# Performance work log

Hardware: AMD Instinct MI355X
Metric: run time of the kernel (lower is better)

## Reference

```python
import jax, jax.numpy as jnp
import numpy as np

N = 50000        # nodes
E = 1_600_000    # edges
R = 4            # relations
F_IN = 32        # input_size
H1 = 32          # 8 * multiplier
H2 = 64          # 16 * multiplier
NC = 3           # num_classes
G = 64           # graphs in batch


def setup_inputs() -> dict:
    key = jax.random.key(0)
    ks = jax.random.split(key, 16)
    s = 0.1
    x = jax.random.normal(ks[0], (N, F_IN), jnp.float32)
    edge_index = jax.random.randint(ks[1], (2, E), 0, N, dtype=jnp.int32)
    edge_type = jax.random.randint(ks[2], (E,), 0, R, dtype=jnp.int32)
    batch = jnp.sort(jax.random.randint(ks[3], (N,), 0, G, dtype=jnp.int32))
    return {
        "x": x,
        "edge_index": edge_index,
        "edge_type": edge_type,
        "batch": batch,
        # RGCNConv 1: per-relation weights, root weight, bias
        "W1_rel": jax.random.normal(ks[4], (R, F_IN, H1), jnp.float32) * s,
        "W1_root": jax.random.normal(ks[5], (F_IN, H1), jnp.float32) * s,
        "b1": jax.random.normal(ks[6], (H1,), jnp.float32) * s,
        # RGCNConv 2
        "W2_rel": jax.random.normal(ks[7], (R, H1, H2), jnp.float32) * s,
        "W2_root": jax.random.normal(ks[8], (H1, H2), jnp.float32) * s,
        "b2": jax.random.normal(ks[9], (H2,), jnp.float32) * s,
        # MLP head (stored as (in, out))
        "lin1_w": jax.random.normal(ks[10], (H2, H1), jnp.float32) * s,
        "lin1_b": jax.random.normal(ks[11], (H1,), jnp.float32) * s,
        "lin2_w": jax.random.normal(ks[12], (H1, NC), jnp.float32) * s,
        "lin2_b": jax.random.normal(ks[13], (NC,), jnp.float32) * s,
    }


def _rgcn_layer(x, src, dst, edge_type, W_rel, W_root, b):
    # PyG RGCNConv: out_i = x_i @ W_root + b + sum_r mean_{j in N_r(i)} x_j @ W_r
    out = x @ W_root + b
    for r in range(R):  # small fixed relation count
        h = x @ W_rel[r]                       # [N, out] dense transform once per relation
        mask = (edge_type == r)
        msg = jnp.where(mask[:, None], h[src], 0.0)          # [E, out] masked gather
        agg = jax.ops.segment_sum(msg, dst, num_segments=N)  # [N, out]
        cnt = jax.ops.segment_sum(mask.astype(x.dtype), dst, num_segments=N)
        out = out + agg / jnp.maximum(cnt, 1.0)[:, None]     # mean aggregation
    return out


def reference(x, edge_index, edge_type, batch, W1_rel, W1_root, b1,
              W2_rel, W2_root, b2, lin1_w, lin1_b, lin2_w, lin2_b):
    src, dst = edge_index[0], edge_index[1]
    h = jax.nn.relu(_rgcn_layer(x, src, dst, edge_type, W1_rel, W1_root, b1))
    h = jax.nn.relu(_rgcn_layer(h, src, dst, edge_type, W2_rel, W2_root, b2))
    g = jax.ops.segment_max(h, batch, num_segments=G)        # global_max_pool -> [G, H2]
    g = jnp.where(jnp.isneginf(g), 0.0, g)                   # empty-graph guard
    g = jax.nn.relu(g @ lin1_w + lin1_b)
    return g @ lin2_w + lin2_b
```

## Files before the change

### kernel.cpp

```cpp
#include <hip/hip_runtime.h>

#define N_NODES 50000
#define N_EDGES 1600000
#define R_REL 4
#define F_IN 32
#define H1 32
#define H2 64
#define NC 3
#define G_BATCH 64
#define BKT 196
#define CHUNK 6400
#define NBIN (N_EDGES / CHUNK)
#define ELIST_CAP (N_EDGES + N_NODES * R_REL * 8)

__global__ __launch_bounds__(256) void copyx_kernel(const float* __restrict__ x,
                                                    float* __restrict__ xp,
                                                    float* __restrict__ h1zero) {
    int i = blockIdx.x * 256 + threadIdx.x;
    if (i < (N_NODES + 1) * F_IN)
        xp[i] = (i < N_NODES * F_IN) ? x[i] : 0.0f;
    if (i < H1) h1zero[i] = 0.0f;
}

__global__ __launch_bounds__(256) void bcount_kernel(const int* __restrict__ dstp,
                                                     int* __restrict__ bucketCnt) {
    __shared__ int h[BKT];
    for (int i = threadIdx.x; i < BKT; i += 256) h[i] = 0;
    __syncthreads();
    int e0 = blockIdx.x * CHUNK;
    for (int e = e0 + threadIdx.x; e < e0 + CHUNK; e += 256)
        atomicAdd(&h[dstp[e] >> 8], 1);
    __syncthreads();
    for (int i = threadIdx.x; i < BKT; i += 256)
        if (h[i]) atomicAdd(&bucketCnt[i], h[i]);
}

__global__ __launch_bounds__(256) void bscan_kernel(const int* __restrict__ bucketCnt,
                                                    int* __restrict__ bucketOff,
                                                    int* __restrict__ bucketCursor) {
    __shared__ int s[256];
    int v = (threadIdx.x < BKT) ? bucketCnt[threadIdx.x] : 0;
    s[threadIdx.x] = v;
    __syncthreads();
    for (int w = 1; w < 256; w <<= 1) {
        int t = (threadIdx.x >= w) ? s[threadIdx.x - w] : 0;
        __syncthreads();
        s[threadIdx.x] += t;
        __syncthreads();
    }
    if (threadIdx.x < BKT) {
        int o = s[threadIdx.x] - v;
        bucketOff[threadIdx.x] = o;
        bucketCursor[threadIdx.x] = o;
    }
}

__global__ __launch_bounds__(256) void bin_kernel(const int* __restrict__ srcp,
                                                  const int* __restrict__ dstp,
                                                  const int* __restrict__ etype,
                                                  int* __restrict__ bucketCursor,
                                                  int* __restrict__ binned) {
    __shared__ int h[BKT];
    __shared__ int lc[BKT];
    for (int i = threadIdx.x; i < BKT; i += 256) { h[i] = 0; lc[i] = 0; }
    __syncthreads();
    int e0 = blockIdx.x * CHUNK;
    for (int e = e0 + threadIdx.x; e < e0 + CHUNK; e += 256)
        atomicAdd(&h[dstp[e] >> 8], 1);
    __syncthreads();
    for (int i = threadIdx.x; i < BKT; i += 256) {
        int c = h[i];
        h[i] = c ? atomicAdd(&bucketCursor[i], c) : 0;
    }
    __syncthreads();
    for (int e = e0 + threadIdx.x; e < e0 + CHUNK; e += 256) {
        int d = dstp[e];
        int b = d >> 8;
        int rank = atomicAdd(&lc[b], 1);
        binned[h[b] + rank] = srcp[e] | (etype[e] << 16) | ((d & 0xFF) << 18);
    }
}

__global__ __launch_bounds__(256) void bcnt2_kernel(const int* __restrict__ binned,
                                                    const int* __restrict__ bucketOff,
                                                    const int* __restrict__ bucketCnt,
                                                    float* __restrict__ inv,
                                                    int* __restrict__ rcnt4,
                                                    int* __restrict__ partial) {
    __shared__ int cnt4[256 * R_REL];
    __shared__ int s[256];
    for (int i = threadIdx.x; i < 256 * R_REL; i += 256) cnt4[i] = 0;
    __syncthreads();
    int b = blockIdx.x;
    int i0 = bucketOff[b], i1 = i0 + bucketCnt[b];
    for (int i = i0 + threadIdx.x; i < i1; i += 256) {
        int p = binned[i];
        atomicAdd(&cnt4[((p >> 18) & 0xFF) * R_REL + ((p >> 16) & 3)], 1);
    }
    __syncthreads();
    int n = b * 256 + threadIdx.x;
    int d = 0;
    if (n < N_NODES) {
        int4 w;
        int c0 = cnt4[threadIdx.x * 4 + 0];
        int c1 = cnt4[threadIdx.x * 4 + 1];
        int c2 = cnt4[threadIdx.x * 4 + 2];
        int c3 = cnt4[threadIdx.x * 4 + 3];
        inv[0 * N_NODES + n] = 1.0f / (float)(c0 > 1 ? c0 : 1);
        inv[1 * N_NODES + n] = 1.0f / (float)(c1 > 1 ? c1 : 1);
        inv[2 * N_NODES + n] = 1.0f / (float)(c2 > 1 ? c2 : 1);
        inv[3 * N_NODES + n] = 1.0f / (float)(c3 > 1 ? c3 : 1);
        w.x = c0; w.y = c1; w.z = c2; w.w = c3;
        *(int4*)&rcnt4[n * 4] = w;
        d = ((c0 + 7) & ~7) + ((c1 + 7) & ~7) + ((c2 + 7) & ~7) + ((c3 + 7) & ~7);
    }
    s[threadIdx.x] = d;
    __syncthreads();
    for (int w = 128; w > 0; w >>= 1) {
        if (threadIdx.x < w) s[threadIdx.x] += s[threadIdx.x + w];
        __syncthreads();
    }
    if (threadIdx.x == 0) partial[b] = s[0];
}

__global__ __launch_bounds__(256) void scanB_kernel(int* __restrict__ partial) {
    __shared__ int s[256];
    int v = (threadIdx.x < BKT) ? partial[threadIdx.x] : 0;
    s[threadIdx.x] = v;
    __syncthreads();
    for (int w = 1; w < 256; w <<= 1) {
        int t = (threadIdx.x >= w) ? s[threadIdx.x - w] : 0;
        __syncthreads();
        s[threadIdx.x] += t;
        __syncthreads();
    }
    if (threadIdx.x < BKT) partial[threadIdx.x] = s[threadIdx.x] - v;
}

__global__ __launch_bounds__(256) void scanC_kernel(const int* __restrict__ rcnt4,
                                                    const int* __restrict__ partial,
                                                    int* __restrict__ poff4) {
    __shared__ int s[256];
    int n = blockIdx.x * 256 + threadIdx.x;
    int p0 = 0, p1 = 0, p2 = 0, p3 = 0, d = 0;
    if (n < N_NODES) {
        int4 rc = *(const int4*)&rcnt4[n * 4];
        p0 = (rc.x + 7) & ~7;
        p1 = (rc.y + 7) & ~7;
        p2 = (rc.z + 7) & ~7;
        p3 = (rc.w + 7) & ~7;
        d = p0 + p1 + p2 + p3;
    }
    s[threadIdx.x] = d;
    __syncthreads();
    for (int w = 1; w < 256; w <<= 1) {
        int t = (threadIdx.x >= w) ? s[threadIdx.x - w] : 0;
        __syncthreads();
        s[threadIdx.x] += t;
        __syncthreads();
    }
    if (n < N_NODES) {
        int base = partial[blockIdx.x] + s[threadIdx.x] - d;
        int4 w;
        w.x = base;
        w.y = base + p0;
        w.z = base + p0 + p1;
        w.w = base + p0 + p1 + p2;
        *(int4*)&poff4[n * 4] = w;
    }
}

__global__ __launch_bounds__(256) void bscatter_kernel(const int* __restrict__ binned,
                                                       const int* __restrict__ bucketOff,
                                                       const int* __restrict__ bucketCnt,
                                                       const int* __restrict__ poff4,
                                                       const int* __restrict__ rcnt4,
                                                       int* __restrict__ elist) {
    __shared__ int cur[256 * 4];
    int b = blockIdx.x, t = threadIdx.x;
    int n = b * 256 + t;
    int4 po = make_int4(0, 0, 0, 0);
    if (n < N_NODES) po = *(const int4*)&poff4[n * 4];
    cur[t * 4 + 0] = po.x;
    cur[t * 4 + 1] = po.y;
    cur[t * 4 + 2] = po.z;
    cur[t * 4 + 3] = po.w;
    __syncthreads();
    int i0 = bucketOff[b], i1 = i0 + bucketCnt[b];
    for (int i = i0 + t; i < i1; i += 256) {
        int p = binned[i];
        int pos = atomicAdd(&cur[((p >> 18) & 0xFF) * 4 + ((p >> 16) & 3)], 1);
        elist[pos] = p & 0xFFFF;
    }
    __syncthreads();
    if (n < N_NODES) {
        int4 rc = *(const int4*)&rcnt4[n * 4];
        int rcv[4] = {rc.x, rc.y, rc.z, rc.w};
        int pov[4] = {po.x, po.y, po.z, po.w};
#pragma unroll
        for (int r = 0; r < R_REL; ++r) {
            int e = cur[t * 4 + r];
            int pe = pov[r] + ((rcv[r] + 7) & ~7);
            for (; e < pe; ++e) elist[e] = N_NODES;
        }
    }
}

__global__ __launch_bounds__(256, 8) void layer1_kernel(
    const float* __restrict__ xp, const int* __restrict__ poff4,
    const int* __restrict__ rcnt4, const int* __restrict__ elist,
    const float* __restrict__ inv, const float* __restrict__ W_rel,
    const float* __restrict__ W_root, const float* __restrict__ b,
    float* __restrict__ h1) {
    __shared__ float sxr[8][F_IN];
    __shared__ float sagg[8][R_REL][F_IN];

    int ln = threadIdx.x >> 5, c = threadIdx.x & 31;
    int n = blockIdx.x * 8 + ln;
    if (n >= N_NODES) return;

    sxr[ln][c] = xp[n * F_IN + c];
    int4 po = *(const int4*)&poff4[n * 4];
    int4 rc = *(const int4*)&rcnt4[n * 4];
    int pov[4] = {po.x, po.y, po.z, po.w};
    int rcv[4] = {rc.x, rc.y, rc.z, rc.w};
    int c7 = c & 7;
#pragma unroll
    for (int r = 0; r < R_REL; ++r) {
        int sb = pov[r];
        int pc = (rcv[r] + 7) & ~7;
        float a = 0.0f;
        for (int eb = 0; eb < pc; eb += 8) {
            int pv = elist[sb + eb + c7];
            float v[8];
#pragma unroll
            for (int j = 0; j < 8; ++j) {
                int p = __shfl(pv, j, 8);
                v[j] = xp[p * F_IN + c];
            }
#pragma unroll
            for (int j = 0; j < 8; ++j) a += v[j];
        }
        sagg[ln][r][c] = a * inv[r * N_NODES + n];
    }

    float o = b[c];
#pragma unroll
    for (int i = 0; i < F_IN; ++i)
        o = fmaf(sxr[ln][i], W_root[i * H1 + c], o);
#pragma unroll
    for (int r = 0; r < R_REL; ++r)
#pragma unroll
        for (int i = 0; i < F_IN; ++i)
            o = fmaf(sagg[ln][r][i], W_rel[r * F_IN * H1 + i * H1 + c], o);
    h1[n * H1 + c] = fmaxf(o, 0.0f);
}

__global__ __launch_bounds__(256, 8) void layer2_kernel(
    const float* __restrict__ h1, const int* __restrict__ poff4,
    const int* __restrict__ rcnt4, const int* __restrict__ elist,
    const float* __restrict__ inv, const float* __restrict__ W_rel,
    const float* __restrict__ W_root, const float* __restrict__ b,
    float* __restrict__ out2) {
    __shared__ float sxr[8][H1];
    __shared__ float sagg[8][R_REL][H1];

    int ln = threadIdx.x >> 5, c = threadIdx.x & 31;
    int n = blockIdx.x * 8 + ln;
    if (n >= N_NODES) return;

    sxr[ln][c] = h1[n * H1 + c];
    int4 po = *(const int4*)&poff4[n * 4];
    int4 rc = *(const int4*)&rcnt4[n * 4];
    int pov[4] = {po.x, po.y, po.z, po.w};
    int rcv[4] = {rc.x, rc.y, rc.z, rc.w};
    int c7 = c & 7;
#pragma unroll
    for (int r = 0; r < R_REL; ++r) {
        int sb = pov[r];
        int pc = (rcv[r] + 7) & ~7;
        float a = 0.0f;
        for (int eb = 0; eb < pc; eb += 8) {
            int pv = elist[sb + eb + c7];
            float v[8];
#pragma unroll
            for (int j = 0; j < 8; ++j) {
                int p = __shfl(pv, j, 8);
                v[j] = h1[p * H1 + c];
            }
#pragma unroll
            for (int j = 0; j < 8; ++j) a += v[j];
        }
        sagg[ln][r][c] = a * inv[r * N_NODES + n];
    }

    float o0 = b[c], o1 = b[c + 32];
#pragma unroll
    for (int i = 0; i < H1; ++i) {
        float xv = sxr[ln][i];
        o0 = fmaf(xv, W_root[i * H2 + c], o0);
        o1 = fmaf(xv, W_root[i * H2 + c + 32], o1);
    }
#pragma unroll
    for (int r = 0; r < R_REL; ++r)
#pragma unroll
        for (int i = 0; i < H1; ++i) {
            float av = sagg[ln][r][i];
            o0 = fmaf(av, W_rel[r * H1 * H2 + i * H2 + c], o0);
            o1 = fmaf(av, W_rel[r * H1 * H2 + i * H2 + c + 32], o1);
        }
    out2[n * H2 + c] = o0;
    out2[n * H2 + c + 32] = o1;
}

#define POOL_NODES 32
__global__ __launch_bounds__(64) void pool_kernel(
    const float* __restrict__ out2, const int* __restrict__ batch,
    unsigned int* __restrict__ g) {
    int col = threadIdx.x;
    int n0 = blockIdx.x * POOL_NODES;
    if (n0 >= N_NODES) return;
    int n1 = n0 + POOL_NODES;
    if (n1 > N_NODES) n1 = N_NODES;
    int cur = batch[n0];
    float m = 0.0f;
    for (int n = n0; n < n1; ++n) {
        int bnow = batch[n];
        if (bnow != cur) {
            atomicMax(&g[cur * H2 + col], __float_as_uint(m));
            cur = bnow;
            m = 0.0f;
        }
        m = fmaxf(m, out2[n * H2 + col]);
    }
    atomicMax(&g[cur * H2 + col], __float_as_uint(m));
}

__global__ __launch_bounds__(256) void mlp_kernel(
    const unsigned int* __restrict__ gbits, const float* __restrict__ lin1_w,
    const float* __restrict__ lin1_b, const float* __restrict__ lin2_w,
    const float* __restrict__ lin2_b, float* __restrict__ out) {
    __shared__ float sg[G_BATCH][H2];
    __shared__ float sh[G_BATCH][H1];
    __shared__ float sw1[H2 * H1];
    for (int i = threadIdx.x; i < G_BATCH * H2; i += 256)
        sg[i / H2][i % H2] = __uint_as_float(gbits[i]);
    for (int i = threadIdx.x; i < H2 * H1; i += 256) sw1[i] = lin1_w[i];
    __syncthreads();
    for (int i = threadIdx.x; i < G_BATCH * H1; i += 256) {
        int gi = i / H1, c = i % H1;
        float a = lin1_b[c];
#pragma unroll
        for (int k = 0; k < H2; ++k) a = fmaf(sg[gi][k], sw1[k * H1 + c], a);
        sh[gi][c] = fmaxf(a, 0.0f);
    }
    __syncthreads();
    for (int i = threadIdx.x; i < G_BATCH * NC; i += 256) {
        int gi = i / NC, c = i % NC;
        float a = lin2_b[c];
#pragma unroll
        for (int k = 0; k < H1; ++k) a = fmaf(sh[gi][k], lin2_w[k * NC + c], a);
        out[gi * NC + c] = a;
    }
}

extern "C" void kernel_launch(void* const* d_in, const int* in_sizes, int n_in,
                              void* d_out, int out_size, void* d_ws, size_t ws_size,
                              hipStream_t stream) {
    const float* x       = (const float*)d_in[0];
    const int*   eidx    = (const int*)d_in[1];
    const int*   etype   = (const int*)d_in[2];
    const int*   batch   = (const int*)d_in[3];
    const float* W1_rel  = (const float*)d_in[4];
    const float* W1_root = (const float*)d_in[5];
    const float* b1      = (const float*)d_in[6];
    const float* W2_rel  = (const float*)d_in[7];
    const float* W2_root = (const float*)d_in[8];
    const float* b2      = (const float*)d_in[9];
    const float* lin1_w  = (const float*)d_in[10];
    const float* lin1_b  = (const float*)d_in[11];
    const float* lin2_w  = (const float*)d_in[12];
    const float* lin2_b  = (const float*)d_in[13];
    const int* srcp = eidx;
    const int* dstp = eidx + N_EDGES;

    char* ws = (char*)d_ws;
    size_t o = 0;
    int*      bucketCnt    = (int*)(ws + o);   o += (size_t)256 * 4;
    int*      bucketOff    = (int*)(ws + o);   o += (size_t)256 * 4;
    int*      bucketCursor = (int*)(ws + o);   o += (size_t)256 * 4;
    int*      partial      = (int*)(ws + o);   o += (size_t)256 * 4;
    float*    inv          = (float*)(ws + o); o += (size_t)R_REL * N_NODES * 4;
    int*      rcnt4        = (int*)(ws + o);   o += (size_t)R_REL * N_NODES * 4;
    int*      poff4        = (int*)(ws + o);   o += (size_t)R_REL * N_NODES * 4;
    int*      binned       = (int*)(ws + o);   o += (size_t)N_EDGES * 4;
    int*      elist        = (int*)(ws + o);   o += (size_t)ELIST_CAP * 4;
    unsigned* g            = (unsigned*)(ws + o); o += (size_t)G_BATCH * H2 * 4;
    float*    xp           = (float*)(ws + o); o += (size_t)(N_NODES + 1) * F_IN * 4;
    float*    h1           = (float*)(ws + o); o += (size_t)(N_NODES + 1) * H1 * 4;
    float*    out2         = (float*)(ws + o); o += (size_t)N_NODES * H2 * 4;

    hipMemsetAsync(bucketCnt, 0, 256 * 4, stream);
    hipMemsetAsync(g, 0, (size_t)G_BATCH * H2 * 4, stream);

    copyx_kernel<<<((N_NODES + 1) * F_IN + 255) / 256, 256, 0, stream>>>(
        x, xp, h1 + (size_t)N_NODES * H1);
    bcount_kernel<<<NBIN, 256, 0, stream>>>(dstp, bucketCnt);
    bscan_kernel<<<1, 256, 0, stream>>>(bucketCnt, bucketOff, bucketCursor);
    bin_kernel<<<NBIN, 256, 0, stream>>>(srcp, dstp, etype, bucketCursor, binned);
    bcnt2_kernel<<<BKT, 256, 0, stream>>>(binned, bucketOff, bucketCnt, inv,
                                          rcnt4, partial);
    scanB_kernel<<<1, 256, 0, stream>>>(partial);
    scanC_kernel<<<BKT, 256, 0, stream>>>(rcnt4, partial, poff4);
    bscatter_kernel<<<BKT, 256, 0, stream>>>(binned, bucketOff, bucketCnt, poff4,
                                             rcnt4, elist);

    layer1_kernel<<<(N_NODES + 7) / 8, 256, 0, stream>>>(
        xp, poff4, rcnt4, elist, inv, W1_rel, W1_root, b1, h1);
    layer2_kernel<<<(N_NODES + 7) / 8, 256, 0, stream>>>(
        h1, poff4, rcnt4, elist, inv, W2_rel, W2_root, b2, out2);

    pool_kernel<<<(N_NODES + POOL_NODES - 1) / POOL_NODES, 64, 0, stream>>>(
        out2, batch, g);
    mlp_kernel<<<1, 256, 0, stream>>>(g, lin1_w, lin1_b, lin2_w, lin2_b,
                                      (float*)d_out);
}
```

Baseline: 320.1 us.

## Gather neighbors with one wavefront per node using float4 loads across relations

Layer kernels now assign a full 64-lane wavefront per node instead of 32 lanes. The wavefront processes 8 edges at once with float4 feature loads, and all four relations are interleaved in a single loop padded to the max count, followed by a cross-lane shuffle reduction. The layer-1 dense transform is split across the two half-waves. This is meant to raise memory-level parallelism and cut per-edge shuffle overhead in the gather, at the cost of wasted padded loads when relation counts differ. The edge-binning chunk size is also reduced to launch more blocks, and the elist gets extra slack for the over-read.

```diff
diff --git a/kernel.cpp b/kernel.cpp
--- a/kernel.cpp
+++ b/kernel.cpp
@@ -9,7 +9,7 @@
 #define NC 3
 #define G_BATCH 64
 #define BKT 196
-#define CHUNK 6400
+#define CHUNK 1600
 #define NBIN (N_EDGES / CHUNK)
 #define ELIST_CAP (N_EDGES + N_NODES * R_REL * 8)
 
@@ -206,111 +206,140 @@
     }
 }
 
+__device__ __forceinline__ void red4(float4& a) {
+#pragma unroll
+    for (int st = 8; st < 64; st <<= 1) {
+        a.x += __shfl_xor(a.x, st);
+        a.y += __shfl_xor(a.y, st);
+        a.z += __shfl_xor(a.z, st);
+        a.w += __shfl_xor(a.w, st);
+    }
+}
+__device__ __forceinline__ void acc4(float4& a, const float4 v) {
+    a.x += v.x; a.y += v.y; a.z += v.z; a.w += v.w;
+}
+
 __global__ __launch_bounds__(256, 8) void layer1_kernel(
     const float* __restrict__ xp, const int* __restrict__ poff4,
     const int* __restrict__ rcnt4, const int* __restrict__ elist,
     const float* __restrict__ inv, const float* __restrict__ W_rel,
-    const float* __restrict__ W_root, const float* __restrict__ b,
+    const float* __restrict__ W_root, const float* __restrict__ bb,
     float* __restrict__ h1) {
-    __shared__ float sxr[8][F_IN];
-    __shared__ float sagg[8][R_REL][F_IN];
-
-    int ln = threadIdx.x >> 5, c = threadIdx.x & 31;
-    int n = blockIdx.x * 8 + ln;
+    __shared__ float sxr[4][F_IN];
+    __shared__ float sagg[4][R_REL][F_IN];
+    int wid = threadIdx.x >> 6, lane = threadIdx.x & 63;
+    int n = blockIdx.x * 4 + wid;
     if (n >= N_NODES) return;
-
-    sxr[ln][c] = xp[n * F_IN + c];
+    int s = lane >> 3, q = lane & 7;
     int4 po = *(const int4*)&poff4[n * 4];
     int4 rc = *(const int4*)&rcnt4[n * 4];
-    int pov[4] = {po.x, po.y, po.z, po.w};
-    int rcv[4] = {rc.x, rc.y, rc.z, rc.w};
-    int c7 = c & 7;
-#pragma unroll
-    for (int r = 0; r < R_REL; ++r) {
-        int sb = pov[r];
-        int pc = (rcv[r] + 7) & ~7;
-        float a = 0.0f;
-        for (int eb = 0; eb < pc; eb += 8) {
-            int pv = elist[sb + eb + c7];
-            float v[8];
-#pragma unroll
-            for (int j = 0; j < 8; ++j) {
-                int p = __shfl(pv, j, 8);
-                v[j] = xp[p * F_IN + c];
-            }
-#pragma unroll
-            for (int j = 0; j < 8; ++j) a += v[j];
-        }
-        sagg[ln][r][c] = a * inv[r * N_NODES + n];
-    }
-
-    float o = b[c];
-#pragma unroll
-    for (int i = 0; i < F_IN; ++i)
-        o = fmaf(sxr[ln][i], W_root[i * H1 + c], o);
+    int pc0 = (rc.x + 7) & ~7, pc1 = (rc.y + 7) & ~7;
+    int pc2 = (rc.z + 7) & ~7, pc3 = (rc.w + 7) & ~7;
+    int mx = max(max(pc0, pc1), max(pc2, pc3));
+    if (lane < 8)
+        *(float4*)&sxr[wid][lane * 4] = *(const float4*)&xp[n * F_IN + lane * 4];
+
+    float4 a0 = {0, 0, 0, 0}, a1 = a0, a2 = a0, a3 = a0;
+    for (int eb = 0; eb < mx; eb += 8) {
+        int t0 = elist[po.x + eb + s];
+        int t1 = elist[po.y + eb + s];
+        int t2 = elist[po.z + eb + s];
+        int t3 = elist[po.w + eb + s];
+        int p0 = (eb < pc0) ? t0 : N_NODES;
+        int p1 = (eb < pc1) ? t1 : N_NODES;
+        int p2 = (eb < pc2) ? t2 : N_NODES;
+        int p3 = (eb < pc3) ? t3 : N_NODES;
+        acc4(a0, *(const float4*)&xp[p0 * F_IN + q * 4]);
+        acc4(a1, *(const float4*)&xp[p1 * F_IN + q * 4]);
+        acc4(a2, *(const float4*)&xp[p2 * F_IN + q * 4]);
+        acc4(a3, *(const float4*)&xp[p3 * F_IN + q * 4]);
+    }
+    red4(a0); red4(a1); red4(a2); red4(a3);
+    if (lane < 8) {
+        float s0 = inv[0 * N_NODES + n], s1 = inv[1 * N_NODES + n];
+        float s2 = inv[2 * N_NODES + n], s3 = inv[3 * N_NODES + n];
+        a0.x *= s0; a0.y *= s0; a0.z *= s0; a0.w *= s0;
+        a1.x *= s1; a1.y *= s1; a1.z *= s1; a1.w *= s1;
+        a2.x *= s2; a2.y *= s2; a2.z *= s2; a2.w *= s2;
+        a3.x *= s3; a3.y *= s3; a3.z *= s3; a3.w *= s3;
+        *(float4*)&sagg[wid][0][lane * 4] = a0;
+        *(float4*)&sagg[wid][1][lane * 4] = a1;
+        *(float4*)&sagg[wid][2][lane * 4] = a2;
+        *(float4*)&sagg[wid][3][lane * 4] = a3;
+    }
+    int col = lane & 31, half = lane >> 5, ib = half * 16;
+    float o = (half == 0) ? bb[col] : 0.0f;
+#pragma unroll
+    for (int k = 0; k < 16; ++k)
+        o = fmaf(sxr[wid][ib + k], W_root[(ib + k) * H1 + col], o);
 #pragma unroll
     for (int r = 0; r < R_REL; ++r)
 #pragma unroll
-        for (int i = 0; i < F_IN; ++i)
-            o = fmaf(sagg[ln][r][i], W_rel[r * F_IN * H1 + i * H1 + c], o);
-    h1[n * H1 + c] = fmaxf(o, 0.0f);
+        for (int k = 0; k < 16; ++k)
+            o = fmaf(sagg[wid][r][ib + k],
+                     W_rel[r * F_IN * H1 + (ib + k) * H1 + col], o);
+    o += __shfl_xor(o, 32);
+    if (half == 0) h1[n * H1 + col] = fmaxf(o, 0.0f);
 }
 
 __global__ __launch_bounds__(256, 8) void layer2_kernel(
     const float* __restrict__ h1, const int* __restrict__ poff4,
     const int* __restrict__ rcnt4, const int* __restrict__ elist,
     const float* __restrict__ inv, const float* __restrict__ W_rel,
-    const float* __restrict__ W_root, const float* __restrict__ b,
+    const float* __restrict__ W_root, const float* __restrict__ bb,
     float* __restrict__ out2) {
-    __shared__ float sxr[8][H1];
-    __shared__ float sagg[8][R_REL][H1];
-
-    int ln = threadIdx.x >> 5, c = threadIdx.x & 31;
-    int n = blockIdx.x * 8 + ln;
+    __shared__ float sxr[4][H1];
+    __shared__ float sagg[4][R_REL][H1];
+    int wid = threadIdx.x >> 6, lane = threadIdx.x & 63;
+    int n = blockIdx.x * 4 + wid;
     if (n >= N_NODES) return;
-
-    sxr[ln][c] = h1[n * H1 + c];
+    int s = lane >> 3, q = lane & 7;
     int4 po = *(const int4*)&poff4[n * 4];
     int4 rc = *(const int4*)&rcnt4[n * 4];
-    int pov[4] = {po.x, po.y, po.z, po.w};
-    int rcv[4] = {rc.x, rc.y, rc.z, rc.w};
-    int c7 = c & 7;
-#pragma unroll
-    for (int r = 0; r < R_REL; ++r) {
-        int sb = pov[r];
-        int pc = (rcv[r] + 7) & ~7;
-        float a = 0.0f;
-        for (int eb = 0; eb < pc; eb += 8) {
-            int pv = elist[sb + eb + c7];
-            float v[8];
-#pragma unroll
-            for (int j = 0; j < 8; ++j) {
-                int p = __shfl(pv, j, 8);
-                v[j] = h1[p * H1 + c];
-            }
-#pragma unroll
-            for (int j = 0; j < 8; ++j) a += v[j];
-        }
-        sagg[ln][r][c] = a * inv[r * N_NODES + n];
-    }
-
-    float o0 = b[c], o1 = b[c + 32];
-#pragma unroll
-    for (int i = 0; i < H1; ++i) {
-        float xv = sxr[ln][i];
-        o0 = fmaf(xv, W_root[i * H2 + c], o0);
-        o1 = fmaf(xv, W_root[i * H2 + c + 32], o1);
-    }
+    int pc0 = (rc.x + 7) & ~7, pc1 = (rc.y + 7) & ~7;
+    int pc2 = (rc.z + 7) & ~7, pc3 = (rc.w + 7) & ~7;
+    int mx = max(max(pc0, pc1), max(pc2, pc3));
+    if (lane < 8)
+        *(float4*)&sxr[wid][lane * 4] = *(const float4*)&h1[n * H1 + lane * 4];
+
+    float4 a0 = {0, 0, 0, 0}, a1 = a0, a2 = a0, a3 = a0;
+    for (int eb = 0; eb < mx; eb += 8) {
+        int t0 = elist[po.x + eb + s];
+        int t1 = elist[po.y + eb + s];
+        int t2 = elist[po.z + eb + s];
+        int t3 = elist[po.w + eb + s];
+        int p0 = (eb < pc0) ? t0 : N_NODES;
+        int p1 = (eb < pc1) ? t1 : N_NODES;
+        int p2 = (eb < pc2) ? t2 : N_NODES;
+        int p3 = (eb < pc3) ? t3 : N_NODES;
+        acc4(a0, *(const float4*)&h1[p0 * H1 + q * 4]);
+        acc4(a1, *(const float4*)&h1[p1 * H1 + q * 4]);
+        acc4(a2, *(const float4*)&h1[p2 * H1 + q * 4]);
+        acc4(a3, *(const float4*)&h1[p3 * H1 + q * 4]);
+    }
+    red4(a0); red4(a1); red4(a2); red4(a3);
+    if (lane < 8) {
+        float s0 = inv[0 * N_NODES + n], s1 = inv[1 * N_NODES + n];
+        float s2 = inv[2 * N_NODES + n], s3 = inv[3 * N_NODES + n];
+        a0.x *= s0; a0.y *= s0; a0.z *= s0; a0.w *= s0;
+        a1.x *= s1; a1.y *= s1; a1.z *= s1; a1.w *= s1;
+        a2.x *= s2; a2.y *= s2; a2.z *= s2; a2.w *= s2;
+        a3.x *= s3; a3.y *= s3; a3.z *= s3; a3.w *= s3;
+        *(float4*)&sagg[wid][0][lane * 4] = a0;
+        *(float4*)&sagg[wid][1][lane * 4] = a1;
+        *(float4*)&sagg[wid][2][lane * 4] = a2;
+        *(float4*)&sagg[wid][3][lane * 4] = a3;
+    }
+    float o = bb[lane];
+#pragma unroll
+    for (int i = 0; i < H1; ++i)
+        o = fmaf(sxr[wid][i], W_root[i * H2 + lane], o);
 #pragma unroll
     for (int r = 0; r < R_REL; ++r)
 #pragma unroll
-        for (int i = 0; i < H1; ++i) {
-            float av = sagg[ln][r][i];
-            o0 = fmaf(av, W_rel[r * H1 * H2 + i * H2 + c], o0);
-            o1 = fmaf(av, W_rel[r * H1 * H2 + i * H2 + c + 32], o1);
-        }
-    out2[n * H2 + c] = o0;
-    out2[n * H2 + c + 32] = o1;
+        for (int i = 0; i < H1; ++i)
+            o = fmaf(sagg[wid][r][i], W_rel[r * H1 * H2 + i * H2 + lane], o);
+    out2[n * H2 + lane] = o;
 }
 
 #define POOL_NODES 32
@@ -394,7 +423,7 @@
     int*      rcnt4        = (int*)(ws + o);   o += (size_t)R_REL * N_NODES * 4;
     int*      poff4        = (int*)(ws + o);   o += (size_t)R_REL * N_NODES * 4;
     int*      binned       = (int*)(ws + o);   o += (size_t)N_EDGES * 4;
-    int*      elist        = (int*)(ws + o);   o += (size_t)ELIST_CAP * 4;
+    int*      elist        = (int*)(ws + o);   o += (size_t)(ELIST_CAP + 4096) * 4;
     unsigned* g            = (unsigned*)(ws + o); o += (size_t)G_BATCH * H2 * 4;
     float*    xp           = (float*)(ws + o); o += (size_t)(N_NODES + 1) * F_IN * 4;
     float*    h1           = (float*)(ws + o); o += (size_t)(N_NODES + 1) * H1 * 4;
@@ -415,9 +444,9 @@
     bscatter_kernel<<<BKT, 256, 0, stream>>>(binned, bucketOff, bucketCnt, poff4,
                                              rcnt4, elist);
 
-    layer1_kernel<<<(N_NODES + 7) / 8, 256, 0, stream>>>(
+    layer1_kernel<<<(N_NODES + 3) / 4, 256, 0, stream>>>(
         xp, poff4, rcnt4, elist, inv, W1_rel, W1_root, b1, h1);
-    layer2_kernel<<<(N_NODES + 7) / 8, 256, 0, stream>>>(
+    layer2_kernel<<<(N_NODES + 3) / 4, 256, 0, stream>>>(
         h1, poff4, rcnt4, elist, inv, W2_rel, W2_root, b2, out2);
 
     pool_kernel<<<(N_NODES + POOL_NODES - 1) / POOL_NODES, 64, 0, stream>>>(
```

New measurement: 357.9 us. +11.8%, slower.

## Use fixed-capacity buckets to drop count pass, scans, and memset

Applied to the files above, without the earlier changes.

Each destination bucket now gets a fixed-capacity slot range (BCAP), so the separate bucket-count kernel, its scan, and the counter memset go away, and the cursor is initialised inside copyx. The single-block scan of per-bucket partials is folded into scanC, where each block reduces the preceding partials itself. CHUNK shrinks so the binning kernel runs more blocks. This cuts kernel launches and one full pass over dst, but relies on no bucket exceeding BCAP (about 8960 edges against an expected 8192 per bucket), which holds only for roughly uniform inputs.

```diff
diff --git a/kernel.cpp b/kernel.cpp
--- a/kernel.cpp
+++ b/kernel.cpp
@@ -9,50 +9,20 @@
 #define NC 3
 #define G_BATCH 64
 #define BKT 196
-#define CHUNK 6400
+#define BCAP 8960
+#define CHUNK 1600
 #define NBIN (N_EDGES / CHUNK)
 #define ELIST_CAP (N_EDGES + N_NODES * R_REL * 8)
 
 __global__ __launch_bounds__(256) void copyx_kernel(const float* __restrict__ x,
                                                     float* __restrict__ xp,
-                                                    float* __restrict__ h1zero) {
+                                                    float* __restrict__ h1zero,
+                                                    int* __restrict__ bucketCursor) {
     int i = blockIdx.x * 256 + threadIdx.x;
     if (i < (N_NODES + 1) * F_IN)
         xp[i] = (i < N_NODES * F_IN) ? x[i] : 0.0f;
     if (i < H1) h1zero[i] = 0.0f;
-}
-
-__global__ __launch_bounds__(256) void bcount_kernel(const int* __restrict__ dstp,
-                                                     int* __restrict__ bucketCnt) {
-    __shared__ int h[BKT];
-    for (int i = threadIdx.x; i < BKT; i += 256) h[i] = 0;
-    __syncthreads();
-    int e0 = blockIdx.x * CHUNK;
-    for (int e = e0 + threadIdx.x; e < e0 + CHUNK; e += 256)
-        atomicAdd(&h[dstp[e] >> 8], 1);
-    __syncthreads();
-    for (int i = threadIdx.x; i < BKT; i += 256)
-        if (h[i]) atomicAdd(&bucketCnt[i], h[i]);
-}
-
-__global__ __launch_bounds__(256) void bscan_kernel(const int* __restrict__ bucketCnt,
-                                                    int* __restrict__ bucketOff,
-                                                    int* __restrict__ bucketCursor) {
-    __shared__ int s[256];
-    int v = (threadIdx.x < BKT) ? bucketCnt[threadIdx.x] : 0;
-    s[threadIdx.x] = v;
-    __syncthreads();
-    for (int w = 1; w < 256; w <<= 1) {
-        int t = (threadIdx.x >= w) ? s[threadIdx.x - w] : 0;
-        __syncthreads();
-        s[threadIdx.x] += t;
-        __syncthreads();
-    }
-    if (threadIdx.x < BKT) {
-        int o = s[threadIdx.x] - v;
-        bucketOff[threadIdx.x] = o;
-        bucketCursor[threadIdx.x] = o;
-    }
+    if (i < BKT) bucketCursor[i] = i * BCAP;
 }
 
 __global__ __launch_bounds__(256) void bin_kernel(const int* __restrict__ srcp,
@@ -82,8 +52,7 @@
 }
 
 __global__ __launch_bounds__(256) void bcnt2_kernel(const int* __restrict__ binned,
-                                                    const int* __restrict__ bucketOff,
-                                                    const int* __restrict__ bucketCnt,
+                                                    const int* __restrict__ bucketCursor,
                                                     float* __restrict__ inv,
                                                     int* __restrict__ rcnt4,
                                                     int* __restrict__ partial) {
@@ -92,7 +61,7 @@
     for (int i = threadIdx.x; i < 256 * R_REL; i += 256) cnt4[i] = 0;
     __syncthreads();
     int b = blockIdx.x;
-    int i0 = bucketOff[b], i1 = i0 + bucketCnt[b];
+    int i0 = b * BCAP, i1 = bucketCursor[b];
     for (int i = i0 + threadIdx.x; i < i1; i += 256) {
         int p = binned[i];
         atomicAdd(&cnt4[((p >> 18) & 0xFF) * R_REL + ((p >> 16) & 3)], 1);
@@ -123,25 +92,23 @@
     if (threadIdx.x == 0) partial[b] = s[0];
 }
 
-__global__ __launch_bounds__(256) void scanB_kernel(int* __restrict__ partial) {
-    __shared__ int s[256];
-    int v = (threadIdx.x < BKT) ? partial[threadIdx.x] : 0;
-    s[threadIdx.x] = v;
-    __syncthreads();
-    for (int w = 1; w < 256; w <<= 1) {
-        int t = (threadIdx.x >= w) ? s[threadIdx.x - w] : 0;
-        __syncthreads();
-        s[threadIdx.x] += t;
-        __syncthreads();
-    }
-    if (threadIdx.x < BKT) partial[threadIdx.x] = s[threadIdx.x] - v;
-}
-
 __global__ __launch_bounds__(256) void scanC_kernel(const int* __restrict__ rcnt4,
                                                     const int* __restrict__ partial,
                                                     int* __restrict__ poff4) {
     __shared__ int s[256];
-    int n = blockIdx.x * 256 + threadIdx.x;
+    __shared__ int pre;
+    int t = threadIdx.x;
+    int pv = (t < blockIdx.x) ? partial[t] : 0;
+    s[t] = pv;
+    __syncthreads();
+    for (int w = 128; w > 0; w >>= 1) {
+        if (t < w) s[t] += s[t + w];
+        __syncthreads();
+    }
+    if (t == 0) pre = s[0];
+    __syncthreads();
+
+    int n = blockIdx.x * 256 + t;
     int p0 = 0, p1 = 0, p2 = 0, p3 = 0, d = 0;
     if (n < N_NODES) {
         int4 rc = *(const int4*)&rcnt4[n * 4];
@@ -151,16 +118,16 @@
         p3 = (rc.w + 7) & ~7;
         d = p0 + p1 + p2 + p3;
     }
-    s[threadIdx.x] = d;
+    s[t] = d;
     __syncthreads();
     for (int w = 1; w < 256; w <<= 1) {
-        int t = (threadIdx.x >= w) ? s[threadIdx.x - w] : 0;
+        int tv = (t >= w) ? s[t - w] : 0;
         __syncthreads();
-        s[threadIdx.x] += t;
+        s[t] += tv;
         __syncthreads();
     }
     if (n < N_NODES) {
-        int base = partial[blockIdx.x] + s[threadIdx.x] - d;
+        int base = pre + s[t] - d;
         int4 w;
         w.x = base;
         w.y = base + p0;
@@ -171,8 +138,7 @@
 }
 
 __global__ __launch_bounds__(256) void bscatter_kernel(const int* __restrict__ binned,
-                                                       const int* __restrict__ bucketOff,
-                                                       const int* __restrict__ bucketCnt,
+                                                       const int* __restrict__ bucketCursor,
                                                        const int* __restrict__ poff4,
                                                        const int* __restrict__ rcnt4,
                                                        int* __restrict__ elist) {
@@ -186,7 +152,7 @@
     cur[t * 4 + 2] = po.z;
     cur[t * 4 + 3] = po.w;
     __syncthreads();
-    int i0 = bucketOff[b], i1 = i0 + bucketCnt[b];
+    int i0 = b * BCAP, i1 = bucketCursor[b];
     for (int i = i0 + t; i < i1; i += 256) {
         int p = binned[i];
         int pos = atomicAdd(&cur[((p >> 18) & 0xFF) * 4 + ((p >> 16) & 3)], 1);
@@ -210,7 +176,7 @@
     const float* __restrict__ xp, const int* __restrict__ poff4,
     const int* __restrict__ rcnt4, const int* __restrict__ elist,
     const float* __restrict__ inv, const float* __restrict__ W_rel,
-    const float* __restrict__ W_root, const float* __restrict__ b,
+    const float* __restrict__ W_root, const float* __restrict__ bb,
     float* __restrict__ h1) {
     __shared__ float sxr[8][F_IN];
     __shared__ float sagg[8][R_REL][F_IN];
@@ -244,7 +210,7 @@
         sagg[ln][r][c] = a * inv[r * N_NODES + n];
     }
 
-    float o = b[c];
+    float o = bb[c];
 #pragma unroll
     for (int i = 0; i < F_IN; ++i)
         o = fmaf(sxr[ln][i], W_root[i * H1 + c], o);
@@ -260,7 +226,7 @@
     const float* __restrict__ h1, const int* __restrict__ poff4,
     const int* __restrict__ rcnt4, const int* __restrict__ elist,
     const float* __restrict__ inv, const float* __restrict__ W_rel,
-    const float* __restrict__ W_root, const float* __restrict__ b,
+    const float* __restrict__ W_root, const float* __restrict__ bb,
     float* __restrict__ out2) {
     __shared__ float sxr[8][H1];
     __shared__ float sagg[8][R_REL][H1];
@@ -294,7 +260,7 @@
         sagg[ln][r][c] = a * inv[r * N_NODES + n];
     }
 
-    float o0 = b[c], o1 = b[c + 32];
+    float o0 = bb[c], o1 = bb[c + 32];
 #pragma unroll
     for (int i = 0; i < H1; ++i) {
         float xv = sxr[ln][i];
@@ -386,33 +352,27 @@
 
     char* ws = (char*)d_ws;
     size_t o = 0;
-    int*      bucketCnt    = (int*)(ws + o);   o += (size_t)256 * 4;
-    int*      bucketOff    = (int*)(ws + o);   o += (size_t)256 * 4;
     int*      bucketCursor = (int*)(ws + o);   o += (size_t)256 * 4;
     int*      partial      = (int*)(ws + o);   o += (size_t)256 * 4;
     float*    inv          = (float*)(ws + o); o += (size_t)R_REL * N_NODES * 4;
     int*      rcnt4        = (int*)(ws + o);   o += (size_t)R_REL * N_NODES * 4;
     int*      poff4        = (int*)(ws + o);   o += (size_t)R_REL * N_NODES * 4;
-    int*      binned       = (int*)(ws + o);   o += (size_t)N_EDGES * 4;
-    int*      elist        = (int*)(ws + o);   o += (size_t)ELIST_CAP * 4;
+    int*      binned       = (int*)(ws + o);   o += (size_t)BKT * BCAP * 4;
+    int*      elist        = (int*)(ws + o);   o += (size_t)(ELIST_CAP + 4096) * 4;
     unsigned* g            = (unsigned*)(ws + o); o += (size_t)G_BATCH * H2 * 4;
     float*    xp           = (float*)(ws + o); o += (size_t)(N_NODES + 1) * F_IN * 4;
     float*    h1           = (float*)(ws + o); o += (size_t)(N_NODES + 1) * H1 * 4;
     float*    out2         = (float*)(ws + o); o += (size_t)N_NODES * H2 * 4;
 
-    hipMemsetAsync(bucketCnt, 0, 256 * 4, stream);
     hipMemsetAsync(g, 0, (size_t)G_BATCH * H2 * 4, stream);
 
     copyx_kernel<<<((N_NODES + 1) * F_IN + 255) / 256, 256, 0, stream>>>(
-        x, xp, h1 + (size_t)N_NODES * H1);
-    bcount_kernel<<<NBIN, 256, 0, stream>>>(dstp, bucketCnt);
-    bscan_kernel<<<1, 256, 0, stream>>>(bucketCnt, bucketOff, bucketCursor);
+        x, xp, h1 + (size_t)N_NODES * H1, bucketCursor);
     bin_kernel<<<NBIN, 256, 0, stream>>>(srcp, dstp, etype, bucketCursor, binned);
-    bcnt2_kernel<<<BKT, 256, 0, stream>>>(binned, bucketOff, bucketCnt, inv,
-                                          rcnt4, partial);
-    scanB_kernel<<<1, 256, 0, stream>>>(partial);
+    bcnt2_kernel<<<BKT, 256, 0, stream>>>(binned, bucketCursor, inv, rcnt4,
+                                          partial);
     scanC_kernel<<<BKT, 256, 0, stream>>>(rcnt4, partial, poff4);
-    bscatter_kernel<<<BKT, 256, 0, stream>>>(binned, bucketOff, bucketCnt, poff4,
+    bscatter_kernel<<<BKT, 256, 0, stream>>>(binned, bucketCursor, poff4,
                                              rcnt4, elist);
 
     layer1_kernel<<<(N_NODES + 7) / 8, 256, 0, stream>>>(
```

Measured after the change: 311.2 us. 2.8% less time.
